# Performance work log

Measured on AMD Instinct MI355X. Metric: run time of the kernel, lower is better.

Reference implementation:

```python
import jax, jax.numpy as jnp
import numpy as np

B, N, S, D = 8, 8192, 4, 256


def setup_inputs() -> dict:
    key = jax.random.key(0)
    kx, kj, kk, k1, k2, k3, k4 = jax.random.split(key, 7)
    x = jax.random.normal(kx, (B, N, D), dtype=jnp.float32)
    ji = jax.random.randint(kj, (B, N, S), 0, N, dtype=jnp.int64)
    ki = jax.random.randint(kk, (B, N, S), 0, N, dtype=jnp.int64)
    # params of nn.Sequential(Linear(3D, D), GELU, Linear(D, D))
    W1 = jax.random.normal(k1, (3 * D, D), dtype=jnp.float32) * 0.02
    b1 = jax.random.normal(k2, (D,), dtype=jnp.float32) * 0.02
    W2 = jax.random.normal(k3, (D, D), dtype=jnp.float32) * 0.02
    b2 = jax.random.normal(k4, (D,), dtype=jnp.float32) * 0.02
    return {"x": x, "ji": ji, "ki": ki, "W1": W1, "b1": b1, "W2": W2, "b2": b2}


def reference(x, ji, ki, W1, b1, W2, b2):
    # gather neighbor features per batch element: [B,N,S,D]
    gather = jax.vmap(lambda xb, ib: xb[ib])
    xj = gather(x, ji)
    xk = gather(x, ki)
    xi = jnp.broadcast_to(x[:, :, None, :], (B, N, S, D))
    h = jnp.concatenate([xi, xj, xk], axis=-1)            # [B,N,S,3D]
    h = jax.nn.gelu(jnp.einsum('bnse,ed->bnsd', h, W1) + b1, approximate=False)
    out = jnp.einsum('bnse,ed->bnsd', h, W2) + b2         # [B,N,S,D]
    return out.mean(axis=2)                               # [B,N,D]
```

## Files before the change

kernel.cpp:

```cpp
#include <hip/hip_runtime.h>
#include <hip/hip_bf16.h>

#define Bb 8
#define Nn 8192
#define Ss 4
#define Dd 256
#define MTOT (Bb*Nn)

typedef unsigned short u16;
typedef short short8 __attribute__((ext_vector_type(8)));
typedef unsigned short u16x4 __attribute__((ext_vector_type(4)));
typedef float f32x4 __attribute__((ext_vector_type(4)));

static __device__ __forceinline__ float bf2f(u16 v) {
  union { unsigned int u; float f; } x; x.u = ((unsigned int)v) << 16; return x.f;
}
static __device__ __forceinline__ u16 f2bf(float f) {
  union { float f; unsigned int u; } x; x.f = f;
  unsigned int u = x.u;
  return (u16)((u + 0x7fffu + ((u >> 16) & 1u)) >> 16);
}

static __device__ __forceinline__ float gelu_fast(float x) {
  float x2 = x * x;
  float z = x * (-2.3021277f - 0.10294456f * x2);
  float e = __builtin_amdgcn_exp2f(z);
  return x * __builtin_amdgcn_rcpf(1.0f + e);
}

__global__ __launch_bounds__(256) void prep_kernel(
    const float* __restrict__ x, const float* __restrict__ W1,
    const float* __restrict__ W2,
    u16* __restrict__ xb, u16* __restrict__ W1t, u16* __restrict__ W2t)
{
  int bid = blockIdx.x, t = threadIdx.x;
  if (bid < 16384) {
    size_t i = ((size_t)bid * 256 + t) * 4;
    f32x4 v = *(const f32x4*)&x[i];
    u16x4 o;
    o[0] = f2bf(v[0]); o[1] = f2bf(v[1]); o[2] = f2bf(v[2]); o[3] = f2bf(v[3]);
    *(u16x4*)&xb[i] = o;
  } else if (bid < 16384 + 768) {
    int j = (bid - 16384) * 256 + t;
    int n = j >> 8, k = j & 255;
    int tb = n >> 8, d = n & 255;
    W1t[j] = f2bf(W1[(size_t)(tb * 256 + k) * 256 + d]);
  } else {
    int j = (bid - 17152) * 256 + t;
    int n = j >> 8, k = j & 255;
    W2t[j] = f2bf(W2[(size_t)k * 256 + n]);
  }
}

template<int MODE, int NBLK>
__global__ __launch_bounds__(256) void gemm128(
    const u16* __restrict__ Ag, const u16* __restrict__ Btg,
    void* __restrict__ Outv, const float* __restrict__ bias, int ldOut)
{
  __shared__ u16 As[128 * 64];
  __shared__ u16 Bs[128 * 64];
  const int t = threadIdx.x;
  const int w = t >> 6, lane = t & 63;
  const int wm = (w >> 1) * 64, wn = (w & 1) * 64;
  const int lr = lane & 15;
  const int lk = (lane >> 4) * 8;

  const int cpx = gridDim.x >> 3;
  const int bid = blockIdx.x;
  const int swz = (bid & 7) * cpx + (bid >> 3);
  const int n0 = (swz % NBLK) * 128;
  const size_t m0 = (size_t)(swz / NBLK) * 128;

  f32x4 acc[4][4];
#pragma unroll
  for (int m = 0; m < 4; ++m)
#pragma unroll
    for (int n = 0; n < 4; ++n)
      acc[m][n] = (f32x4){0.f, 0.f, 0.f, 0.f};

  for (int kt = 0; kt < 4; ++kt) {
#pragma unroll
    for (int pass = 0; pass < 4; ++pass) {
      int c = pass * 256 + t;
      int row = c >> 3, cc = c & 7;
      int scc = cc ^ (row & 7);
      const u16* ga = Ag + (m0 + row) * 256 + kt * 64 + scc * 8;
      u16* la = As + pass * 2048 + (t & 192) * 8;
      __builtin_amdgcn_global_load_lds(
          (const __attribute__((address_space(1))) void*)ga,
          (__attribute__((address_space(3))) void*)la, 16, 0, 0);
      const u16* gb = Btg + (size_t)(n0 + row) * 256 + kt * 64 + scc * 8;
      u16* lb = Bs + pass * 2048 + (t & 192) * 8;
      __builtin_amdgcn_global_load_lds(
          (const __attribute__((address_space(1))) void*)gb,
          (__attribute__((address_space(3))) void*)lb, 16, 0, 0);
    }
    __syncthreads();
#pragma unroll
    for (int kk = 0; kk < 2; ++kk) {
      short8 af[4], bfr[4];
#pragma unroll
      for (int m = 0; m < 4; ++m) {
        int rA = wm + m * 16 + lr;
        af[m] = *(const short8*)&As[(rA * 64 + kk * 32 + lk) ^ ((rA & 7) << 3)];
      }
#pragma unroll
      for (int n = 0; n < 4; ++n) {
        int rB = wn + n * 16 + lr;
        bfr[n] = *(const short8*)&Bs[(rB * 64 + kk * 32 + lk) ^ ((rB & 7) << 3)];
      }
#pragma unroll
      for (int m = 0; m < 4; ++m)
#pragma unroll
        for (int n = 0; n < 4; ++n)
          acc[m][n] = __builtin_amdgcn_mfma_f32_16x16x32_bf16(
              af[m], bfr[n], acc[m][n], 0, 0, 0);
    }
    __syncthreads();
  }

#pragma unroll
  for (int m = 0; m < 4; ++m) {
    int rbase = wm + m * 16 + ((lane >> 4) << 2);
#pragma unroll
    for (int n = 0; n < 4; ++n) {
      int col = n0 + wn + n * 16 + (lane & 15);
#pragma unroll
      for (int rr = 0; rr < 4; ++rr) {
        size_t row = m0 + rbase + rr;
        if (MODE == 0) {
          ((u16*)Outv)[row * (size_t)ldOut + col] = f2bf(acc[m][n][rr]);
        } else {
          ((float*)Outv)[row * (size_t)ldOut + col] = acc[m][n][rr] + bias[col];
        }
      }
    }
  }
}

__global__ __launch_bounds__(256) void gather_gelu_mean(
    const u16* __restrict__ ABC, const int* __restrict__ ji,
    const int* __restrict__ ki, const float* __restrict__ b1,
    u16* __restrict__ Hm)
{
  int t = threadIdx.x, w = t >> 6, lane = t & 63;
  size_t r = (size_t)blockIdx.x * 4 + w;
  int base = ((int)(r >> 13)) << 13;
  int d0 = lane * 4;

  f32x4 bias = *(const f32x4*)&b1[d0];
  u16x4 av = *(const u16x4*)(ABC + r * 768 + d0);
  float a0 = bf2f(av[0]) + bias[0];
  float a1 = bf2f(av[1]) + bias[1];
  float a2 = bf2f(av[2]) + bias[2];
  float a3 = bf2f(av[3]) + bias[3];

  const int* jr = ji + r * 4;
  const int* kr = ki + r * 4;
  float acc0 = 0.f, acc1 = 0.f, acc2 = 0.f, acc3 = 0.f;
#pragma unroll
  for (int s = 0; s < 4; ++s) {
    size_t gj = (size_t)(base + jr[s]);
    size_t gk = (size_t)(base + kr[s]);
    u16x4 bv = *(const u16x4*)(ABC + gj * 768 + 256 + d0);
    u16x4 cv = *(const u16x4*)(ABC + gk * 768 + 512 + d0);
    float x0 = a0 + bf2f(bv[0]) + bf2f(cv[0]);
    float x1 = a1 + bf2f(bv[1]) + bf2f(cv[1]);
    float x2 = a2 + bf2f(bv[2]) + bf2f(cv[2]);
    float x3 = a3 + bf2f(bv[3]) + bf2f(cv[3]);
    acc0 += gelu_fast(x0);
    acc1 += gelu_fast(x1);
    acc2 += gelu_fast(x2);
    acc3 += gelu_fast(x3);
  }
  u16x4 hv;
  hv[0] = f2bf(acc0 * 0.25f);
  hv[1] = f2bf(acc1 * 0.25f);
  hv[2] = f2bf(acc2 * 0.25f);
  hv[3] = f2bf(acc3 * 0.25f);
  *(u16x4*)(Hm + r * 256 + d0) = hv;
}

extern "C" void kernel_launch(void* const* d_in, const int* in_sizes, int n_in,
                              void* d_out, int out_size, void* d_ws, size_t ws_size,
                              hipStream_t stream) {
  (void)in_sizes; (void)n_in; (void)out_size; (void)ws_size;
  const float* x  = (const float*)d_in[0];
  const int*   ji = (const int*)d_in[1];
  const int*   ki = (const int*)d_in[2];
  const float* W1 = (const float*)d_in[3];
  const float* b1 = (const float*)d_in[4];
  const float* W2 = (const float*)d_in[5];
  const float* b2 = (const float*)d_in[6];
  float* out = (float*)d_out;

  char* ws = (char*)d_ws;
  u16* xb  = (u16*)ws;  ws += (size_t)MTOT * 256 * 2;
  u16* ABC = (u16*)ws;  ws += (size_t)MTOT * 768 * 2;
  u16* Hm  = (u16*)ws;  ws += (size_t)MTOT * 256 * 2;
  u16* W1t = (u16*)ws;  ws += 768 * 256 * 2;
  u16* W2t = (u16*)ws;  ws += 256 * 256 * 2;

  prep_kernel<<<17408, 256, 0, stream>>>(x, W1, W2, xb, W1t, W2t);

  gemm128<0, 6><<<(MTOT / 128) * 6, 256, 0, stream>>>(
      xb, W1t, (void*)ABC, nullptr, 768);

  gather_gelu_mean<<<MTOT / 4, 256, 0, stream>>>(ABC, ji, ki, b1, Hm);

  gemm128<1, 2><<<(MTOT / 128) * 2, 256, 0, stream>>>(
      Hm, W2t, (void*)out, b2, 256);
}
```

Measured before the change: 122.3 us.

## Fuse gather-GELU-mean with second GEMM using LDS-resident hidden tile

The gather/GELU/mean step now writes its 64-row hidden tile into shared memory instead of global memory, and the same block then runs the W2 GEMM with MFMA and writes the biased fp32 output. This removes the intermediate Hm buffer's global write and read and one kernel launch. In exchange, each block uses a large LDS footprint that limits occupancy for the latency-bound gather phase. W2 is also streamed repeatedly per block without double buffering.

```diff
diff --git a/kernel.cpp b/kernel.cpp
--- a/kernel.cpp
+++ b/kernel.cpp
@@ -52,10 +52,10 @@
   }
 }
 
-template<int MODE, int NBLK>
+template<int NBLK>
 __global__ __launch_bounds__(256) void gemm128(
     const u16* __restrict__ Ag, const u16* __restrict__ Btg,
-    void* __restrict__ Outv, const float* __restrict__ bias, int ldOut)
+    u16* __restrict__ Out, int ldOut)
 {
   __shared__ u16 As[128 * 64];
   __shared__ u16 Bs[128 * 64];
@@ -128,57 +128,135 @@
 #pragma unroll
       for (int rr = 0; rr < 4; ++rr) {
         size_t row = m0 + rbase + rr;
-        if (MODE == 0) {
-          ((u16*)Outv)[row * (size_t)ldOut + col] = f2bf(acc[m][n][rr]);
-        } else {
-          ((float*)Outv)[row * (size_t)ldOut + col] = acc[m][n][rr] + bias[col];
-        }
-      }
-    }
-  }
-}
-
-__global__ __launch_bounds__(256) void gather_gelu_mean(
+        Out[row * (size_t)ldOut + col] = f2bf(acc[m][n][rr]);
+      }
+    }
+  }
+}
+
+__global__ __launch_bounds__(256) void gather_gemm2(
     const u16* __restrict__ ABC, const int* __restrict__ ji,
     const int* __restrict__ ki, const float* __restrict__ b1,
-    u16* __restrict__ Hm)
+    const u16* __restrict__ W2t, const float* __restrict__ b2,
+    float* __restrict__ out)
 {
-  int t = threadIdx.x, w = t >> 6, lane = t & 63;
-  size_t r = (size_t)blockIdx.x * 4 + w;
-  int base = ((int)(r >> 13)) << 13;
-  int d0 = lane * 4;
+  __shared__ u16 Hs[64 * 256];
+  __shared__ u16 W2s[256 * 64];
+  const int t = threadIdx.x;
+  const int w = t >> 6, lane = t & 63;
+  const size_t r0 = (size_t)blockIdx.x * 64;
+  const int base = ((int)(r0 >> 13)) << 13;
+  const int d0 = lane * 4;
+
+#pragma unroll
+  for (int pass = 0; pass < 8; ++pass) {
+    int c = pass * 256 + t;
+    int n = c >> 3, cc = c & 7;
+    int scc = cc ^ (n & 7);
+    const u16* g = W2t + n * 256 + scc * 8;
+    u16* l = W2s + pass * 2048 + (t & 192) * 8;
+    __builtin_amdgcn_global_load_lds(
+        (const __attribute__((address_space(1))) void*)g,
+        (__attribute__((address_space(3))) void*)l, 16, 0, 0);
+  }
 
   f32x4 bias = *(const f32x4*)&b1[d0];
-  u16x4 av = *(const u16x4*)(ABC + r * 768 + d0);
-  float a0 = bf2f(av[0]) + bias[0];
-  float a1 = bf2f(av[1]) + bias[1];
-  float a2 = bf2f(av[2]) + bias[2];
-  float a3 = bf2f(av[3]) + bias[3];
-
-  const int* jr = ji + r * 4;
-  const int* kr = ki + r * 4;
-  float acc0 = 0.f, acc1 = 0.f, acc2 = 0.f, acc3 = 0.f;
-#pragma unroll
-  for (int s = 0; s < 4; ++s) {
-    size_t gj = (size_t)(base + jr[s]);
-    size_t gk = (size_t)(base + kr[s]);
-    u16x4 bv = *(const u16x4*)(ABC + gj * 768 + 256 + d0);
-    u16x4 cv = *(const u16x4*)(ABC + gk * 768 + 512 + d0);
-    float x0 = a0 + bf2f(bv[0]) + bf2f(cv[0]);
-    float x1 = a1 + bf2f(bv[1]) + bf2f(cv[1]);
-    float x2 = a2 + bf2f(bv[2]) + bf2f(cv[2]);
-    float x3 = a3 + bf2f(bv[3]) + bf2f(cv[3]);
-    acc0 += gelu_fast(x0);
-    acc1 += gelu_fast(x1);
-    acc2 += gelu_fast(x2);
-    acc3 += gelu_fast(x3);
-  }
-  u16x4 hv;
-  hv[0] = f2bf(acc0 * 0.25f);
-  hv[1] = f2bf(acc1 * 0.25f);
-  hv[2] = f2bf(acc2 * 0.25f);
-  hv[3] = f2bf(acc3 * 0.25f);
-  *(u16x4*)(Hm + r * 256 + d0) = hv;
+  for (int it = 0; it < 16; ++it) {
+    int row = w * 16 + it;
+    size_t r = r0 + row;
+    u16x4 av = *(const u16x4*)(ABC + r * 768 + d0);
+    float a0 = bf2f(av[0]) + bias[0];
+    float a1 = bf2f(av[1]) + bias[1];
+    float a2 = bf2f(av[2]) + bias[2];
+    float a3 = bf2f(av[3]) + bias[3];
+    const int* jr = ji + r * 4;
+    const int* kr = ki + r * 4;
+    float acc0 = 0.f, acc1 = 0.f, acc2 = 0.f, acc3 = 0.f;
+#pragma unroll
+    for (int s = 0; s < 4; ++s) {
+      size_t gj = (size_t)(base + jr[s]);
+      size_t gk = (size_t)(base + kr[s]);
+      u16x4 bv = *(const u16x4*)(ABC + gj * 768 + 256 + d0);
+      u16x4 cv = *(const u16x4*)(ABC + gk * 768 + 512 + d0);
+      float x0 = a0 + bf2f(bv[0]) + bf2f(cv[0]);
+      float x1 = a1 + bf2f(bv[1]) + bf2f(cv[1]);
+      float x2 = a2 + bf2f(bv[2]) + bf2f(cv[2]);
+      float x3 = a3 + bf2f(bv[3]) + bf2f(cv[3]);
+      acc0 += gelu_fast(x0);
+      acc1 += gelu_fast(x1);
+      acc2 += gelu_fast(x2);
+      acc3 += gelu_fast(x3);
+    }
+    u16x4 hv;
+    hv[0] = f2bf(acc0 * 0.25f);
+    hv[1] = f2bf(acc1 * 0.25f);
+    hv[2] = f2bf(acc2 * 0.25f);
+    hv[3] = f2bf(acc3 * 0.25f);
+    *(u16x4*)&Hs[(row * 256 + d0) ^ ((row & 7) << 3)] = hv;
+  }
+  __syncthreads();
+
+  const int wm = (w >> 1) * 32, wn = (w & 1) * 128;
+  const int lr = lane & 15, lk = (lane >> 4) * 8;
+  f32x4 acc[2][8];
+#pragma unroll
+  for (int m = 0; m < 2; ++m)
+#pragma unroll
+    for (int n = 0; n < 8; ++n)
+      acc[m][n] = (f32x4){0.f, 0.f, 0.f, 0.f};
+
+  for (int kt = 0; kt < 4; ++kt) {
+#pragma unroll
+    for (int kk = 0; kk < 2; ++kk) {
+      short8 af[2], bfr[8];
+#pragma unroll
+      for (int m = 0; m < 2; ++m) {
+        int rA = wm + m * 16 + lr;
+        af[m] = *(const short8*)&Hs[(rA * 256 + kt * 64 + kk * 32 + lk) ^ ((rA & 7) << 3)];
+      }
+#pragma unroll
+      for (int n = 0; n < 8; ++n) {
+        int rB = wn + n * 16 + lr;
+        bfr[n] = *(const short8*)&W2s[(rB * 64 + kk * 32 + lk) ^ ((rB & 7) << 3)];
+      }
+#pragma unroll
+      for (int m = 0; m < 2; ++m)
+#pragma unroll
+        for (int n = 0; n < 8; ++n)
+          acc[m][n] = __builtin_amdgcn_mfma_f32_16x16x32_bf16(
+              af[m], bfr[n], acc[m][n], 0, 0, 0);
+    }
+    __syncthreads();
+    if (kt < 3) {
+#pragma unroll
+      for (int pass = 0; pass < 8; ++pass) {
+        int c = pass * 256 + t;
+        int n = c >> 3, cc = c & 7;
+        int scc = cc ^ (n & 7);
+        const u16* g = W2t + n * 256 + (kt + 1) * 64 + scc * 8;
+        u16* l = W2s + pass * 2048 + (t & 192) * 8;
+        __builtin_amdgcn_global_load_lds(
+            (const __attribute__((address_space(1))) void*)g,
+            (__attribute__((address_space(3))) void*)l, 16, 0, 0);
+      }
+      __syncthreads();
+    }
+  }
+
+#pragma unroll
+  for (int m = 0; m < 2; ++m) {
+    int rbase = wm + m * 16 + ((lane >> 4) << 2);
+#pragma unroll
+    for (int n = 0; n < 8; ++n) {
+      int col = wn + n * 16 + lr;
+      float bb = b2[col];
+#pragma unroll
+      for (int rr = 0; rr < 4; ++rr) {
+        size_t row = r0 + rbase + rr;
+        out[row * 256 + col] = acc[m][n][rr] + bb;
+      }
+    }
+  }
 }
 
 extern "C" void kernel_launch(void* const* d_in, const int* in_sizes, int n_in,
@@ -197,17 +275,12 @@
   char* ws = (char*)d_ws;
   u16* xb  = (u16*)ws;  ws += (size_t)MTOT * 256 * 2;
   u16* ABC = (u16*)ws;  ws += (size_t)MTOT * 768 * 2;
-  u16* Hm  = (u16*)ws;  ws += (size_t)MTOT * 256 * 2;
   u16* W1t = (u16*)ws;  ws += 768 * 256 * 2;
   u16* W2t = (u16*)ws;  ws += 256 * 256 * 2;
 
   prep_kernel<<<17408, 256, 0, stream>>>(x, W1, W2, xb, W1t, W2t);
 
-  gemm128<0, 6><<<(MTOT / 128) * 6, 256, 0, stream>>>(
-      xb, W1t, (void*)ABC, nullptr, 768);
-
-  gather_gelu_mean<<<MTOT / 4, 256, 0, stream>>>(ABC, ji, ki, b1, Hm);
-
-  gemm128<1, 2><<<(MTOT / 128) * 2, 256, 0, stream>>>(
-      Hm, W2t, (void*)out, b2, 256);
-}
+  gemm128<6><<<(MTOT / 128) * 6, 256, 0, stream>>>(xb, W1t, ABC, 768);
+
+  gather_gemm2<<<MTOT / 64, 256, 0, stream>>>(ABC, ji, ki, b1, W2t, b2, out);
+}
```

Result: faster. 119.6 us (-2.2%).
